# Kernel optimization log

Hardware: AMD Instinct MI355X
Metric: run time of the kernel (lower is better)

The kernel has to match this reference:

```python
import jax, jax.numpy as jnp
import numpy as np

FD, FO, FK, H = 1024, 512, 128, 4
N = 32768


def setup_inputs() -> dict:
    key = jax.random.key(0)
    ks = jax.random.split(key, 8)
    s = 0.02
    return {
        "Xd": jax.random.normal(ks[0], (N, FD), dtype=jnp.float32),
        "Xo": jax.random.normal(ks[1], (N, FO), dtype=jnp.float32),
        "Wq": jax.random.normal(ks[2], (FO, FK * H), dtype=jnp.float32) * s,
        "bq": jnp.zeros((FK * H,), dtype=jnp.float32),
        "Wk": jax.random.normal(ks[3], (FD, FK * H), dtype=jnp.float32) * s,
        "bk": jnp.zeros((FK * H,), dtype=jnp.float32),
        "Wv": jax.random.normal(ks[4], (FD, FD * H), dtype=jnp.float32) * s,
        "bv": jnp.zeros((FD * H,), dtype=jnp.float32),
    }


def reference(Xd, Xo, Wq, bq, Wk, bk, Wv, bv):
    n = Xd.shape[0]
    Q = (Xo @ Wq + bq).reshape(n, H, FK)      # (n, H, fk)
    K = (Xd @ Wk + bk).reshape(n, H, FK)      # (n, H, fk)
    V = (Xd @ Wv + bv).reshape(n, H, FD)      # (n, H, fd)
    scores = jnp.sum(Q * K, axis=2, keepdims=True)  # (n, H, 1), no softmax
    Z = scores * V                              # (n, H, fd)
    Z = jnp.max(Z, axis=1)                      # max pooling over heads -> (n, fd)
    return Z  # dropout is identity in inference
```

## Files before the change

### kernel.cpp

```cpp
#include <hip/hip_runtime.h>

typedef __attribute__((ext_vector_type(8))) short short8;
typedef __attribute__((ext_vector_type(4))) float f32x4;

#define GLL16(gp, lp) __builtin_amdgcn_global_load_lds( \
    (__attribute__((address_space(1))) void*)(gp), \
    (__attribute__((address_space(3))) void*)(lp), 16, 0, 0)

__device__ __forceinline__ unsigned short f2b(float f) {
  unsigned int u = __builtin_bit_cast(unsigned int, f);
  u += 0x7fffu + ((u >> 16) & 1u);
  return (unsigned short)(u >> 16);
}
__device__ __forceinline__ float b2f(unsigned short s) {
  unsigned int u = ((unsigned int)s) << 16;
  return __builtin_bit_cast(float, u);
}

__global__ __launch_bounds__(256) void conv_k(const float* __restrict__ in,
                                              short8* __restrict__ out, long n8) {
  for (long i = (long)blockIdx.x * 256 + threadIdx.x; i < n8;
       i += (long)gridDim.x * 256) {
    const float4* p = (const float4*)in + 2 * i;
    float4 a = p[0], b = p[1];
    short8 v;
    v[0] = (short)f2b(a.x); v[1] = (short)f2b(a.y);
    v[2] = (short)f2b(a.z); v[3] = (short)f2b(a.w);
    v[4] = (short)f2b(b.x); v[5] = (short)f2b(b.y);
    v[6] = (short)f2b(b.z); v[7] = (short)f2b(b.w);
    out[i] = v;
  }
}

__global__ __launch_bounds__(256) void tconv_k(const float* __restrict__ in,
                                               unsigned short* __restrict__ out,
                                               int K, int C, int inter) {
  __shared__ float t[32][33];
  int k0 = blockIdx.x * 32, c0 = blockIdx.y * 32;
  int tx = threadIdx.x & 31, ty = threadIdx.x >> 5;
#pragma unroll
  for (int p = 0; p < 4; ++p)
    t[ty + p * 8][tx] = in[(size_t)(k0 + ty + p * 8) * C + c0 + tx];
  __syncthreads();
#pragma unroll
  for (int p = 0; p < 4; ++p) {
    int c = ty + p * 8;
    int gc = c0 + c;
    int orow = inter ? ((gc & 1023) * 4 + (gc >> 10)) : gc;
    out[(size_t)orow * K + k0 + tx] = f2b(t[tx][c]);
  }
}

template <int KD, int NTI, int EPI>
__global__ __launch_bounds__(512, 2) void gemm_p(
    const unsigned short* __restrict__ A, const unsigned short* __restrict__ Bt,
    const float* __restrict__ bias, const unsigned short* __restrict__ Qb,
    unsigned short* __restrict__ outb, float* __restrict__ sc,
    float* __restrict__ Z) {
  __shared__ __align__(16) char lds[131072];
  __shared__ float s_sc[1024];

  constexpr int NKT = KD / 64;
  int tid = threadIdx.x;
  int bid = blockIdx.x;
  int cpx = gridDim.x >> 3;
  int lb = (bid & 7) * cpx + (bid >> 3);
  int mtile = lb / NTI, nt0 = lb % NTI;
  long m0 = (long)mtile * 256;
  int l = tid & 63, wid = tid >> 6, wm = wid >> 2, wn = wid & 3;

  int rowg = tid >> 3;
  int swz = (tid & 7) ^ (rowg & 7);
  const char* aSrc = (const char*)(A + m0 * KD) + (long)rowg * (KD * 2) + swz * 16;
  const char* bSrc = (const char*)(Bt + (long)nt0 * 256 * KD) + (long)rowg * (KD * 2) + swz * 16;
  char* ldsb = (char*)lds;
  int dstOff = wid * 1024;

  auto stageA = [&](int hh, int tt) {
    char* base = ldsb + ((tt & 1) * 32768 + hh * 16384) + dstOff;
    const char* s = aSrc + (long)(hh * 128) * (KD * 2) + tt * 128;
    GLL16(s, base);
    GLL16(s + (long)64 * (KD * 2), base + 8192);
  };
  auto stageB = [&](int hh, int tt) {
    char* base = ldsb + 65536 + ((tt & 1) * 32768 + hh * 16384) + dstOff;
    const char* s = bSrc + (long)(hh * 128) * (KD * 2) + tt * 128;
    GLL16(s, base);
    GLL16(s + (long)64 * (KD * 2), base + 8192);
  };

  int ar = l & 15, kcl = l >> 4;
  int x0 = ((kcl ^ (ar & 7)) << 4);
  int x1 = (((4 | kcl) ^ (ar & 7)) << 4);
  int thrA = (wm * 64 + ar) * 128;
  int thrB = (wn * 32 + ar) * 128;

  short8 aA[4][2], aB[4][2], b0[2][2], b1[2][2];

#define RD_A(dst, slotoff)                                                  \
  do {                                                                      \
    const char* p_ = ldsb + (slotoff) + thrA;                               \
    _Pragma("unroll") for (int m_ = 0; m_ < 4; ++m_) {                      \
      dst[m_][0] = *(const short8*)(p_ + x0 + m_ * 2048);                   \
      dst[m_][1] = *(const short8*)(p_ + x1 + m_ * 2048);                   \
    }                                                                       \
  } while (0)
#define RD_B(dst, slotoff)                                                  \
  do {                                                                      \
    const char* p_ = ldsb + 65536 + (slotoff) + thrB;                       \
    _Pragma("unroll") for (int n_ = 0; n_ < 2; ++n_) {                      \
      dst[n_][0] = *(const short8*)(p_ + x0 + n_ * 2048);                   \
      dst[n_][1] = *(const short8*)(p_ + x1 + n_ * 2048);                   \
    }                                                                       \
  } while (0)
#define MFQ(q, am, bn)                                                      \
  do {                                                                      \
    __builtin_amdgcn_s_setprio(1);                                          \
    _Pragma("unroll") for (int m_ = 0; m_ < 4; ++m_)                        \
        _Pragma("unroll") for (int n_ = 0; n_ < 2; ++n_)                    \
            _Pragma("unroll") for (int k_ = 0; k_ < 2; ++k_)                \
                acc[q][m_ * 2 + n_] = __builtin_amdgcn_mfma_f32_16x16x32_bf16( \
                    am[m_][k_], bn[n_][k_], acc[q][m_ * 2 + n_], 0, 0, 0);  \
    __builtin_amdgcn_s_setprio(0);                                          \
  } while (0)
#define VM(n) asm volatile("s_waitcnt vmcnt(" #n ")" ::: "memory")
#define BAR() __builtin_amdgcn_s_barrier()
#define CLOB() asm volatile("" ::: "memory")

  f32x4 zero = {0.f, 0.f, 0.f, 0.f};
  f32x4 acc[4][8];
#pragma unroll
  for (int q = 0; q < 4; ++q)
#pragma unroll
    for (int f = 0; f < 8; ++f) acc[q][f] = zero;

  stageA(0, 0); stageB(0, 0); stageB(1, 0); stageA(1, 0);
  if constexpr (EPI == 2) {
    for (int i = tid; i < 1024; i += 512) s_sc[i] = sc[m0 * 4 + i];
  }
  VM(4); BAR(); CLOB();
  RD_A(aA, 0);
  RD_B(b0, 0);

  for (int t = 0; t < NKT - 1; ++t) {
    int aS = (t & 1) * 32768;
    int bS = aS;
    int aS2 = aS ^ 32768;
    stageA(0, t + 1);
    VM(4); BAR(); CLOB();
    RD_B(b1, bS + 16384);
    MFQ(0, aA, b0);
    stageB(0, t + 1);
    VM(4); BAR(); CLOB();
    RD_A(aB, aS + 16384);
    MFQ(1, aA, b1);
    stageB(1, t + 1);
    VM(4); BAR(); CLOB();
    RD_A(aA, aS2);
    MFQ(2, aB, b0);
    stageA(1, t + 1);
    VM(4); BAR(); CLOB();
    RD_B(b0, aS2);
    MFQ(3, aB, b1);
  }
  {
    constexpr int t = NKT - 1;
    int aS = (t & 1) * 32768;
    VM(2); BAR(); CLOB();
    RD_B(b1, aS + 16384);
    MFQ(0, aA, b0);
    VM(0); BAR(); CLOB();
    RD_A(aB, aS + 16384);
    MFQ(1, aA, b1);
    MFQ(2, aB, b0);
    MFQ(3, aB, b1);
  }
#undef RD_A
#undef RD_B
#undef MFQ
#undef VM
#undef BAR
#undef CLOB

  if constexpr (EPI == 0) {
#pragma unroll
    for (int qm = 0; qm < 2; ++qm)
#pragma unroll
      for (int qn = 0; qn < 2; ++qn) {
        int q = qm * 2 + qn;
#pragma unroll
        for (int n = 0; n < 2; ++n) {
          int col = nt0 * 256 + qn * 128 + wn * 32 + n * 16 + (l & 15);
          float bb = bias[col];
#pragma unroll
          for (int m = 0; m < 4; ++m) {
            long rowb = m0 + qm * 128 + wm * 64 + m * 16 + ((l >> 4) << 2);
#pragma unroll
            for (int r = 0; r < 4; ++r)
              outb[(rowb + r) * 512 + col] = f2b(acc[q][m * 2 + n][r] + bb);
          }
        }
      }
  } else if constexpr (EPI == 1) {
    float part[2][2][4][4];
#pragma unroll
    for (int qm = 0; qm < 2; ++qm)
#pragma unroll
      for (int qn = 0; qn < 2; ++qn)
#pragma unroll
        for (int m = 0; m < 4; ++m)
#pragma unroll
          for (int r = 0; r < 4; ++r) part[qm][qn][m][r] = 0.f;
#pragma unroll
    for (int qm = 0; qm < 2; ++qm)
#pragma unroll
      for (int qn = 0; qn < 2; ++qn) {
        int q = qm * 2 + qn;
#pragma unroll
        for (int n = 0; n < 2; ++n) {
          int col = nt0 * 256 + qn * 128 + wn * 32 + n * 16 + (l & 15);
          float bb = bias[col];
#pragma unroll
          for (int m = 0; m < 4; ++m) {
            long rowb = m0 + qm * 128 + wm * 64 + m * 16 + ((l >> 4) << 2);
#pragma unroll
            for (int r = 0; r < 4; ++r) {
              float kv = acc[q][m * 2 + n][r] + bb;
              part[qm][qn][m][r] += kv * b2f(Qb[(rowb + r) * 512 + col]);
            }
          }
        }
      }
    __syncthreads();
    float (*sred)[2][4] = (float(*)[2][4])ldsb;
#pragma unroll
    for (int qm = 0; qm < 2; ++qm)
#pragma unroll
      for (int qn = 0; qn < 2; ++qn)
#pragma unroll
        for (int m = 0; m < 4; ++m)
#pragma unroll
          for (int r = 0; r < 4; ++r) {
            float s = part[qm][qn][m][r];
            s += __shfl_xor(s, 1);
            s += __shfl_xor(s, 2);
            s += __shfl_xor(s, 4);
            s += __shfl_xor(s, 8);
            if ((l & 15) == 0)
              sred[qm * 128 + wm * 64 + m * 16 + ((l >> 4) << 2) + r][qn][wn] = s;
          }
    __syncthreads();
    {
      int row = tid >> 1, hh = tid & 1;
      float v = sred[row][hh][0] + sred[row][hh][1] + sred[row][hh][2] +
                sred[row][hh][3];
      sc[(m0 + row) * 4 + nt0 * 2 + hh] = v;
    }
  } else {
    __syncthreads();
    float* Zs = (float*)ldsb;
#pragma unroll
    for (int qm = 0; qm < 2; ++qm)
#pragma unroll
      for (int qn = 0; qn < 2; ++qn) {
        int q = qm * 2 + qn;
#pragma unroll
        for (int n = 0; n < 2; ++n) {
          int pl = qn * 128 + wn * 32 + n * 16 + (l & 15);
          int pg = nt0 * 256 + pl;
          int h = pl & 3;
          float bb = bias[(pg & 3) * 1024 + (pg >> 2)];
#pragma unroll
          for (int m = 0; m < 4; ++m) {
            int rl = qm * 128 + wm * 64 + m * 16 + ((l >> 4) << 2);
#pragma unroll
            for (int r = 0; r < 4; ++r) {
              float z = s_sc[(rl + r) * 4 + h] * (acc[q][m * 2 + n][r] + bb);
              z = fmaxf(z, __shfl_xor(z, 1));
              z = fmaxf(z, __shfl_xor(z, 2));
              if ((l & 3) == 0) Zs[(rl + r) * 64 + (pl >> 2)] = z;
            }
          }
        }
      }
    __syncthreads();
#pragma unroll
    for (int it = 0; it < 8; ++it) {
      int i = it * 512 + tid;
      int row = i >> 4, d4 = i & 15;
      f32x4 v = *(const f32x4*)&Zs[row * 64 + d4 * 4];
      *(f32x4*)&Z[(m0 + row) * 1024 + nt0 * 64 + d4 * 4] = v;
    }
  }
}

__global__ __launch_bounds__(256) void naive_k(
    const float* __restrict__ Xd, const float* __restrict__ Xo,
    const float* __restrict__ Wq, const float* __restrict__ bq,
    const float* __restrict__ Wk, const float* __restrict__ bk,
    const float* __restrict__ Wv, const float* __restrict__ bv,
    float* __restrict__ Z) {
  int i = blockIdx.x, t = threadIdx.x;
  __shared__ float xd[1024], xo[512], s[4];
  for (int j = t; j < 1024; j += 256) xd[j] = Xd[(size_t)i * 1024 + j];
  for (int j = t; j < 512; j += 256) xo[j] = Xo[(size_t)i * 512 + j];
  if (t < 4) s[t] = 0.f;
  __syncthreads();
  for (int c = t; c < 512; c += 256) {
    float q = bq[c], k = bk[c];
    for (int j = 0; j < 512; ++j) q += xo[j] * Wq[(size_t)j * 512 + c];
    for (int j = 0; j < 1024; ++j) k += xd[j] * Wk[(size_t)j * 512 + c];
    atomicAdd(&s[c >> 7], q * k);
  }
  __syncthreads();
  for (int d = t; d < 1024; d += 256) {
    float z = -INFINITY;
    for (int h = 0; h < 4; ++h) {
      float v = bv[h * 1024 + d];
      for (int j = 0; j < 1024; ++j) v += xd[j] * Wv[(size_t)j * 4096 + h * 1024 + d];
      z = fmaxf(z, s[h] * v);
    }
    Z[(size_t)i * 1024 + d] = z;
  }
}

extern "C" void kernel_launch(void* const* d_in, const int* in_sizes, int n_in,
                              void* d_out, int out_size, void* d_ws, size_t ws_size,
                              hipStream_t stream) {
  const float* Xd = (const float*)d_in[0];
  const float* Xo = (const float*)d_in[1];
  const float* Wq = (const float*)d_in[2];
  const float* bq = (const float*)d_in[3];
  const float* Wk = (const float*)d_in[4];
  const float* bk = (const float*)d_in[5];
  const float* Wv = (const float*)d_in[6];
  const float* bv = (const float*)d_in[7];
  float* Z = (float*)d_out;
  long N = in_sizes[0] / 1024;

  size_t sz_Xd = (size_t)N * 1024 * 2, sz_Xo = (size_t)N * 512 * 2;
  size_t sz_Wq = (size_t)512 * 512 * 2, sz_Wk = (size_t)512 * 1024 * 2;
  size_t sz_Wv = (size_t)4096 * 1024 * 2;
  size_t sz_Qb = (size_t)N * 512 * 2, sz_sc = (size_t)N * 4 * 4;
  size_t o_Xo = sz_Xd, o_Wq = o_Xo + sz_Xo, o_Wk = o_Wq + sz_Wq,
         o_Wv = o_Wk + sz_Wk, o_Qb = o_Wv + sz_Wv, o_sc = o_Qb + sz_Qb;
  size_t need = o_sc + sz_sc;

  if (ws_size < need || (N % 256) != 0) {
    naive_k<<<(int)N, 256, 0, stream>>>(Xd, Xo, Wq, bq, Wk, bk, Wv, bv, Z);
    return;
  }

  char* w = (char*)d_ws;
  unsigned short* Xd_b = (unsigned short*)w;
  unsigned short* Xo_b = (unsigned short*)(w + o_Xo);
  unsigned short* Wq_t = (unsigned short*)(w + o_Wq);
  unsigned short* Wk_t = (unsigned short*)(w + o_Wk);
  unsigned short* Wv_p = (unsigned short*)(w + o_Wv);
  unsigned short* Qb   = (unsigned short*)(w + o_Qb);
  float* sc = (float*)(w + o_sc);

  conv_k<<<2048, 256, 0, stream>>>(Xd, (short8*)Xd_b, N * 1024 / 8);
  conv_k<<<2048, 256, 0, stream>>>(Xo, (short8*)Xo_b, N * 512 / 8);
  tconv_k<<<dim3(16, 16), 256, 0, stream>>>(Wq, Wq_t, 512, 512, 0);
  tconv_k<<<dim3(32, 16), 256, 0, stream>>>(Wk, Wk_t, 1024, 512, 0);
  tconv_k<<<dim3(32, 128), 256, 0, stream>>>(Wv, Wv_p, 1024, 4096, 1);

  int mt = (int)(N / 256);
  gemm_p<512, 2, 0><<<mt * 2, 512, 0, stream>>>(Xo_b, Wq_t, bq, nullptr, Qb,
                                                nullptr, nullptr);
  gemm_p<1024, 2, 1><<<mt * 2, 512, 0, stream>>>(Xd_b, Wk_t, bk, Qb, nullptr,
                                                 sc, nullptr);
  gemm_p<1024, 16, 2><<<mt * 16, 512, 0, stream>>>(Xd_b, Wv_p, bv, nullptr,
                                                   nullptr, sc, Z);
}
```

Before: 471.3 us.

## Replace V-projection GEMM with smaller-tile triple-buffered kernel for higher occupancy

The dominant V GEMM with its score-scale and head-max epilogue now runs in a new kernel using 256x128 output tiles, a 32-wide K step and a three-stage LDS ring. The LDS footprint drops from 128KB to about 72KB so more blocks can be resident per CU. The launch count doubles to mt*32 blocks. In exchange it gives up the larger 256x256 tile's operand reuse and adds more barriers per K step, and the simpler pipeline has less fine-grained interleaving of loads and MFMAs. The old EPI==2 path is removed from gemm_p.

```diff
diff --git a/kernel.cpp b/kernel.cpp
--- a/kernel.cpp
+++ b/kernel.cpp
@@ -51,14 +51,121 @@
   }
 }
 
+template <int KD>
+__global__ __launch_bounds__(512, 4) void gemm_v2(
+    const unsigned short* __restrict__ A, const unsigned short* __restrict__ Bt,
+    const float* __restrict__ bias, const float* __restrict__ sc,
+    float* __restrict__ Z) {
+  __shared__ __align__(16) char lds[73728];
+  __shared__ float s_sc[1024];
+
+  constexpr int NKT = KD / 32;
+  int tid = threadIdx.x;
+  int bid = blockIdx.x;
+  int cpx = gridDim.x >> 3;
+  int lb = (bid & 7) * cpx + (bid >> 3);
+  int mtile = lb >> 5, nt0 = lb & 31;
+  long m0 = (long)mtile * 256;
+  int l = tid & 63, wid = tid >> 6, wm = wid >> 1, wn = wid & 1;
+
+  int srg = tid >> 3, slot = tid & 7;
+  int se = slot ^ (srg & 7);
+  int par = se >> 2, kc = se & 3;
+  int rowb = srg * 2 + par;
+  const char* aT = (const char*)(A + m0 * KD) + (long)rowb * (KD * 2) + kc * 16;
+  const char* bT = (const char*)(Bt + (long)nt0 * 128 * KD) + (long)rowb * (KD * 2) + kc * 16;
+  char* ldsb = (char*)lds;
+  int dstOff = wid * 1024;
+
+  auto stage = [&](int kt, int bb) {
+    int ko = kt * 64;
+    GLL16(aT + ko,                  ldsb + bb * 24576 + dstOff);
+    GLL16(aT + 128 * (KD * 2) + ko, ldsb + bb * 24576 + 8192 + dstOff);
+    GLL16(bT + ko,                  ldsb + bb * 24576 + 16384 + dstOff);
+  };
+
+  for (int i = tid; i < 1024; i += 512) s_sc[i] = sc[m0 * 4 + i];
+
+  int ar = l & 15, kcl = l >> 4;
+  int aoffR[4], boffR[4];
+#pragma unroll
+  for (int m = 0; m < 4; ++m) {
+    int wr = wm * 64 + m * 16 + ar, sr = wr >> 1;
+    aoffR[m] = sr * 128 + (((((wr & 1) << 2) | kcl) ^ (sr & 7)) << 4);
+  }
+#pragma unroll
+  for (int n = 0; n < 4; ++n) {
+    int br = wn * 64 + n * 16 + ar, sr = br >> 1;
+    boffR[n] = 16384 + sr * 128 + (((((br & 1) << 2) | kcl) ^ (sr & 7)) << 4);
+  }
+
+  f32x4 zero = {0.f, 0.f, 0.f, 0.f};
+  f32x4 acc[4][4];
+#pragma unroll
+  for (int m = 0; m < 4; ++m)
+#pragma unroll
+    for (int n = 0; n < 4; ++n) acc[m][n] = zero;
+
+  stage(0, 0);
+  stage(1, 1);
+
+  for (int t = 0; t < NKT; ++t) {
+    if (t + 1 < NKT) asm volatile("s_waitcnt vmcnt(3)" ::: "memory");
+    else             asm volatile("s_waitcnt vmcnt(0)" ::: "memory");
+    __builtin_amdgcn_s_barrier();
+    asm volatile("" ::: "memory");
+    if (t + 2 < NKT) stage(t + 2, (t + 2) % 3);
+
+    const char* base = ldsb + (t % 3) * 24576;
+    short8 af[4], bf[4];
+#pragma unroll
+    for (int m = 0; m < 4; ++m) af[m] = *(const short8*)(base + aoffR[m]);
+#pragma unroll
+    for (int n = 0; n < 4; ++n) bf[n] = *(const short8*)(base + boffR[n]);
+#pragma unroll
+    for (int m = 0; m < 4; ++m)
+#pragma unroll
+      for (int n = 0; n < 4; ++n)
+        acc[m][n] = __builtin_amdgcn_mfma_f32_16x16x32_bf16(af[m], bf[n],
+                                                            acc[m][n], 0, 0, 0);
+  }
+
+  __syncthreads();
+  float* Zs = (float*)ldsb;
+#pragma unroll
+  for (int n = 0; n < 4; ++n) {
+    int pl = wn * 64 + n * 16 + (l & 15);
+    int pg = nt0 * 128 + pl;
+    int h = pl & 3;
+    float bb = bias[(pg & 3) * 1024 + (pg >> 2)];
+#pragma unroll
+    for (int m = 0; m < 4; ++m) {
+      int rl = wm * 64 + m * 16 + ((l >> 4) << 2);
+#pragma unroll
+      for (int r = 0; r < 4; ++r) {
+        float z = s_sc[(rl + r) * 4 + h] * (acc[m][n][r] + bb);
+        z = fmaxf(z, __shfl_xor(z, 1));
+        z = fmaxf(z, __shfl_xor(z, 2));
+        if ((l & 3) == 0) Zs[(rl + r) * 32 + (pl >> 2)] = z;
+      }
+    }
+  }
+  __syncthreads();
+#pragma unroll
+  for (int it = 0; it < 4; ++it) {
+    int i = it * 512 + tid;
+    int row = i >> 3, q = i & 7;
+    f32x4 v = *(const f32x4*)&Zs[row * 32 + q * 4];
+    *(f32x4*)&Z[(m0 + row) * 1024 + nt0 * 32 + q * 4] = v;
+  }
+}
+
 template <int KD, int NTI, int EPI>
 __global__ __launch_bounds__(512, 2) void gemm_p(
     const unsigned short* __restrict__ A, const unsigned short* __restrict__ Bt,
     const float* __restrict__ bias, const unsigned short* __restrict__ Qb,
-    unsigned short* __restrict__ outb, float* __restrict__ sc,
-    float* __restrict__ Z) {
+    unsigned short* __restrict__ outb, float* __restrict__ sc) {
   __shared__ __align__(16) char lds[131072];
-  __shared__ float s_sc[1024];
 
   constexpr int NKT = KD / 64;
   int tid = threadIdx.x;
@@ -135,9 +242,6 @@
     for (int f = 0; f < 8; ++f) acc[q][f] = zero;
 
   stageA(0, 0); stageB(0, 0); stageB(1, 0); stageA(1, 0);
-  if constexpr (EPI == 2) {
-    for (int i = tid; i < 1024; i += 512) s_sc[i] = sc[m0 * 4 + i];
-  }
   VM(4); BAR(); CLOB();
   RD_A(aA, 0);
   RD_B(b0, 0);
@@ -201,7 +305,7 @@
           }
         }
       }
-  } else if constexpr (EPI == 1) {
+  } else {
     float part[2][2][4][4];
 #pragma unroll
     for (int qm = 0; qm < 2; ++qm)
@@ -255,41 +359,6 @@
       float v = sred[row][hh][0] + sred[row][hh][1] + sred[row][hh][2] +
                 sred[row][hh][3];
       sc[(m0 + row) * 4 + nt0 * 2 + hh] = v;
-    }
-  } else {
-    __syncthreads();
-    float* Zs = (float*)ldsb;
-#pragma unroll
-    for (int qm = 0; qm < 2; ++qm)
-#pragma unroll
-      for (int qn = 0; qn < 2; ++qn) {
-        int q = qm * 2 + qn;
-#pragma unroll
-        for (int n = 0; n < 2; ++n) {
-          int pl = qn * 128 + wn * 32 + n * 16 + (l & 15);
-          int pg = nt0 * 256 + pl;
-          int h = pl & 3;
-          float bb = bias[(pg & 3) * 1024 + (pg >> 2)];
-#pragma unroll
-          for (int m = 0; m < 4; ++m) {
-            int rl = qm * 128 + wm * 64 + m * 16 + ((l >> 4) << 2);
-#pragma unroll
-            for (int r = 0; r < 4; ++r) {
-              float z = s_sc[(rl + r) * 4 + h] * (acc[q][m * 2 + n][r] + bb);
-              z = fmaxf(z, __shfl_xor(z, 1));
-              z = fmaxf(z, __shfl_xor(z, 2));
-              if ((l & 3) == 0) Zs[(rl + r) * 64 + (pl >> 2)] = z;
-            }
-          }
-        }
-      }
-    __syncthreads();
-#pragma unroll
-    for (int it = 0; it < 8; ++it) {
-      int i = it * 512 + tid;
-      int row = i >> 4, d4 = i & 15;
-      f32x4 v = *(const f32x4*)&Zs[row * 64 + d4 * 4];
-      *(f32x4*)&Z[(m0 + row) * 1024 + nt0 * 64 + d4 * 4] = v;
     }
   }
 }
@@ -368,9 +437,8 @@
 
   int mt = (int)(N / 256);
   gemm_p<512, 2, 0><<<mt * 2, 512, 0, stream>>>(Xo_b, Wq_t, bq, nullptr, Qb,
-                                                nullptr, nullptr);
+                                                nullptr);
   gemm_p<1024, 2, 1><<<mt * 2, 512, 0, stream>>>(Xd_b, Wk_t, bk, Qb, nullptr,
-                                                 sc, nullptr);
-  gemm_p<1024, 16, 2><<<mt * 16, 512, 0, stream>>>(Xd_b, Wv_p, bv, nullptr,
-                                                   nullptr, sc, Z);
-}
+                                                 sc);
+  gemm_v2<1024><<<mt * 32, 512, 0, stream>>>(Xd_b, Wv_p, bv, sc, Z);
+}
```

Measured after the change: 472.1 us. About the same (+0.2%).
